# Kernel optimization log

Measured on AMD Instinct MI355X. Metric: run time of the kernel, lower is better.

The kernel has to match this reference:

```python
import jax, jax.numpy as jnp
import numpy as np

K = 20
EPS = 1e-5
NUM_CLASSES = 50


def knn_idx(x, k):
    # x: [B, C, N] -> [B, N, k] indices of k nearest neighbors (self included)
    xx = jnp.sum(x * x, axis=1)                      # [B, N]
    inner = jnp.einsum('bcn,bcm->bnm', x, x)         # [B, N, N]
    neg_dist = 2.0 * inner - xx[:, :, None] - xx[:, None, :]
    return jax.lax.top_k(neg_dist, k)[1]


def graph_feature(x, k):
    # x: [B, C, N] -> [B, 2C, N, k] edge features (feat - center, center)
    B = x.shape[0]
    idx = knn_idx(x, k)                              # [B, N, k]
    xt = jnp.transpose(x, (0, 2, 1))                 # [B, N, C]
    feat = xt[jnp.arange(B)[:, None, None], idx]     # [B, N, k, C]
    center = xt[:, :, None, :]
    out = jnp.concatenate([feat - center, jnp.broadcast_to(center, feat.shape)], axis=-1)
    return jnp.transpose(out, (0, 3, 1, 2))


def group_norm(x, groups, w, b):
    B, C = x.shape[0], x.shape[1]
    shp = x.shape
    xg = x.reshape(B, groups, -1)
    mu = jnp.mean(xg, axis=-1, keepdims=True)
    var = jnp.var(xg, axis=-1, keepdims=True)
    xn = ((xg - mu) * jax.lax.rsqrt(var + EPS)).reshape(shp)
    bshape = (1, C) + (1,) * (len(shp) - 2)
    return xn * w.reshape(bshape) + b.reshape(bshape)


def leaky(x):
    return jnp.where(x >= 0, x, 0.2 * x)


def edge_block(x, W, gw, gb, groups, k):
    f = graph_feature(x, k)                          # [B, 2C, N, k]
    h = jnp.einsum('oc,bcnk->bonk', W, f)            # 1x1 conv2d, no bias
    h = leaky(group_norm(h, groups, gw, gb))
    return jnp.max(h, axis=-1)                       # [B, Cout, N]


def conv1d(x, W, b):
    return jnp.einsum('oc,bcn->bon', W, x) + b[None, :, None]


def _mk(key, shape, fan_in):
    return jax.random.normal(key, shape, jnp.float32) * (1.0 / np.sqrt(fan_in))


def setup_inputs():
    key = jax.random.key(0)
    ks = jax.random.split(key, 32)
    B, N = 8, 2048
    d = {}
    d['x'] = jax.random.normal(ks[0], (B, 3, N), jnp.float32)
    d['W1'] = _mk(ks[1], (64, 6), 6)
    d['W2'] = _mk(ks[2], (64, 128), 128)
    d['W3'] = _mk(ks[3], (128, 128), 128)
    for i, (name, c) in enumerate([('g1', 64), ('g2', 64), ('g3', 128), ('gf', 1024), ('gs1', 512), ('gs2', 256), ('gs3', 128)]):
        d[name + 'w'] = 1.0 + 0.02 * jax.random.normal(ks[4 + 2 * i], (c,), jnp.float32)
        d[name + 'b'] = 0.02 * jax.random.normal(ks[5 + 2 * i], (c,), jnp.float32)
    d['Wm'] = _mk(ks[20], (1024, 256), 256)
    d['bm'] = jnp.zeros((1024,), jnp.float32)
    d['Ws1'] = _mk(ks[21], (512, 1280), 1280)
    d['bs1'] = jnp.zeros((512,), jnp.float32)
    d['Ws2'] = _mk(ks[22], (256, 512), 512)
    d['bs2'] = jnp.zeros((256,), jnp.float32)
    d['Ws3'] = _mk(ks[23], (128, 256), 256)
    d['bs3'] = jnp.zeros((128,), jnp.float32)
    d['Ws4'] = _mk(ks[24], (NUM_CLASSES, 128), 128)
    d['bs4'] = jnp.zeros((NUM_CLASSES,), jnp.float32)
    return d


def reference(x, W1, W2, W3, g1w, g1b, g2w, g2b, g3w, g3b, gfw, gfb, gs1w, gs1b, gs2w, gs2b, gs3w, gs3b, Wm, bm, Ws1, bs1, Ws2, bs2, Ws3, bs3, Ws4, bs4):
    B, _, N = x.shape
    x1 = edge_block(x, W1, g1w, g1b, 8, K)           # [B, 64, N]
    x2 = edge_block(x1, W2, g2w, g2b, 8, K)          # [B, 64, N]
    x3 = edge_block(x2, W3, g3w, g3b, 8, K)          # [B, 128, N]
    feats = jnp.concatenate([x1, x2, x3], axis=1)    # [B, 256, N]
    xb = jax.nn.relu(group_norm(conv1d(feats, Wm, bm), 32, gfw, gfb))  # [B, 1024, N]
    xmax = jnp.max(xb, axis=2)                       # [B, 1024]
    xmax_exp = jnp.broadcast_to(xmax[:, :, None], (B, 1024, N))
    combined = jnp.concatenate([xmax_exp, feats], axis=1)  # [B, 1280, N]
    h = jax.nn.relu(group_norm(conv1d(combined, Ws1, bs1), 16, gs1w, gs1b))
    h = jax.nn.relu(group_norm(conv1d(h, Ws2, bs2), 16, gs2w, gs2b))
    h = jax.nn.relu(group_norm(conv1d(h, Ws3, bs3), 8, gs3w, gs3b))
    logits = conv1d(h, Ws4, bs4)                     # [B, num_classes, N]
    return jax.nn.log_softmax(logits, axis=1)
```

## Files before the change

### kernel.cpp

```cpp
#include <hip/hip_runtime.h>

#define BN 8
#define NP 2048
#define KK 20
#define EPSV 1e-5f

typedef __attribute__((ext_vector_type(8))) short bf16x8;
typedef __attribute__((ext_vector_type(4))) float f32x4;

static __device__ __forceinline__ float leakyf(float v){ return v >= 0.f ? v : 0.2f*v; }
static __device__ __forceinline__ unsigned fenc(float f){
  unsigned u = __float_as_uint(f);
  unsigned m = (unsigned)((int)u >> 31);
  return u ^ (m | 0x80000000u);
}
static __device__ __forceinline__ float fdec(unsigned u){
  return __uint_as_float((u & 0x80000000u) ? (u & 0x7FFFFFFFu) : ~u);
}
static __device__ __forceinline__ unsigned bf2(float a, float b){
  unsigned ua = __float_as_uint(a), ub = __float_as_uint(b);
  ua = (ua + 0x7FFFu + ((ua>>16)&1u)) >> 16;
  ub = (ub + 0x7FFFu + ((ub>>16)&1u)) >> 16;
  return ua | (ub<<16);
}
static __device__ __forceinline__ unsigned short b16(float v){
  unsigned u = __float_as_uint(v);
  return (unsigned short)((u + 0x7FFFu + ((u>>16)&1u)) >> 16);
}
static __device__ __forceinline__ unsigned umax32(unsigned a, unsigned b){ return __builtin_elementwise_max(a,b); }
static __device__ __forceinline__ unsigned med3u(unsigned a, unsigned b, unsigned c){
  unsigned d;
  asm("v_med3_u32 %0, %1, %2, %3" : "=v"(d) : "v"(a), "v"(b), "v"(c));
  return d;
}

static __device__ __forceinline__ char* ldsW(char* base, int row, int colb){
  return base + row*80 + (colb ^ ((((unsigned)row>>3)&3u)<<4));
}
static __device__ __forceinline__ char* ldsX(char* base, int row, int colb){
  return base + row*80 + (colb ^ (((((unsigned)row>>2)^((unsigned)row>>4))&3u)<<4));
}
static __device__ __forceinline__ int swz128(int row, int colb){
  return (colb ^ ((row&7)<<4));
}

__global__ __launch_bounds__(256) void xx_kernel(const float* __restrict__ x, long ldb, int C,
                                                 float* __restrict__ xx){
  int b = blockIdx.y;
  int n = blockIdx.x*256 + threadIdx.x;
  const float* xp = x + (long)b*ldb + n;
  float a = 0.f;
  for(int c=0;c<C;c++){ float v = xp[(long)c*NP]; a += v*v; }
  xx[b*NP + n] = a;
}

static __device__ __forceinline__ void ins20(unsigned* tv, unsigned key){
  unsigned pold = tv[0];
  tv[0] = umax32(tv[0], key);
  #pragma unroll
  for(int r=1;r<20;r++){
    unsigned cold = tv[r];
    tv[r] = med3u(key, pold, cold);
    pold = cold;
  }
}

__global__ __launch_bounds__(256) void knnf_kernel(const unsigned short* __restrict__ fh,
                                                   const unsigned short* __restrict__ fl,
                                                   const float* __restrict__ xx,
                                                   unsigned* __restrict__ pk){
  __shared__ unsigned short CH[64][68];
  __shared__ unsigned short CL[64][68];
  __shared__ unsigned SK[64][68];
  __shared__ float cxs[64];
  const int b    = blockIdx.z;
  const int part = blockIdx.y;
  const int q0   = blockIdx.x*64;
  const int t    = threadIdx.x;
  const int lane = t & 63;
  const int w    = t >> 6;
  const int lr   = lane & 15, lg = lane >> 4;
  const unsigned short* fhb = fh + (long)b*NP*64;
  const unsigned short* flb = fl + (long)b*NP*64;
  const float* xxb = xx + b*NP;

  const unsigned short* qa = fhb + ((long)(q0 + w*16 + lr))*64 + lg*8;
  const unsigned short* qb = flb + ((long)(q0 + w*16 + lr))*64 + lg*8;
  bf16x8 ah0 = *(const bf16x8*)(qa);
  bf16x8 ah1 = *(const bf16x8*)(qa + 32);
  bf16x8 al0 = *(const bf16x8*)(qb);
  bf16x8 al1 = *(const bf16x8*)(qb + 32);
  float4 qxx4 = *(const float4*)(xxb + q0 + w*16 + lg*4);
  float qxx[4] = {qxx4.x, qxx4.y, qxx4.z, qxx4.w};

  unsigned tv[20];
  #pragma unroll
  for(int r=0;r<20;r++) tv[r] = 0u;
  const int sq = t>>2, sl = t&3;

  #define STAGE(ct_)                                                                  \
    {                                                                                 \
      const int ct__ = (ct_);                                                         \
      _Pragma("unroll")                                                               \
      for(int i = t; i < 512; i += 256){                                              \
        int row = i >> 3, seg = i & 7;                                                \
        *(uint4*)&CH[row][seg*8] = *(const uint4*)(fhb + ((long)(ct__*64+row))*64 + seg*8); \
        *(uint4*)&CL[row][seg*8] = *(const uint4*)(flb + ((long)(ct__*64+row))*64 + seg*8); \
      }                                                                               \
      if (t < 64) cxs[t] = xxb[ct__*64 + t];                                          \
    }

  STAGE(part*4);
  __syncthreads();

  #pragma unroll
  for(int cc=0; cc<4; cc++){
    __builtin_amdgcn_s_setprio(1);
    f32x4 acc[4];
    #pragma unroll
    for(int nt=0; nt<4; nt++){
      int crow = nt*16 + lr;
      bf16x8 bh0 = *(const bf16x8*)&CH[crow][lg*8];
      bf16x8 bh1 = *(const bf16x8*)&CH[crow][32 + lg*8];
      bf16x8 bl0 = *(const bf16x8*)&CL[crow][lg*8];
      bf16x8 bl1 = *(const bf16x8*)&CL[crow][32 + lg*8];
      f32x4 a = (f32x4){0.f,0.f,0.f,0.f};
      a = __builtin_amdgcn_mfma_f32_16x16x32_bf16(ah0, bh0, a, 0,0,0);
      a = __builtin_amdgcn_mfma_f32_16x16x32_bf16(ah1, bh1, a, 0,0,0);
      a = __builtin_amdgcn_mfma_f32_16x16x32_bf16(ah0, bl0, a, 0,0,0);
      a = __builtin_amdgcn_mfma_f32_16x16x32_bf16(ah1, bl1, a, 0,0,0);
      a = __builtin_amdgcn_mfma_f32_16x16x32_bf16(al0, bh0, a, 0,0,0);
      a = __builtin_amdgcn_mfma_f32_16x16x32_bf16(al1, bh1, a, 0,0,0);
      acc[nt] = a;
    }
    __builtin_amdgcn_s_setprio(0);
    float cxv[4];
    #pragma unroll
    for(int nt=0; nt<4; nt++) cxv[nt] = cxs[nt*16 + lr];
    unsigned key4[4][4];
    #pragma unroll
    for(int nt=0; nt<4; nt++){
      #pragma unroll
      for(int r=0;r<4;r++){
        float neg = 2.f*acc[nt][r] - qxx[r] - cxv[nt];
        key4[nt][r] = (fenc(neg) & 0xFFFFFF00u) | (255u - (unsigned)(cc*64 + nt*16 + lr));
      }
    }
    __syncthreads();
    #pragma unroll
    for(int nt=0; nt<4; nt++)
      #pragma unroll
      for(int r=0;r<4;r++)
        SK[w*16 + lg*4 + r][nt*16 + lr] = key4[nt][r];
    if (cc < 3){
      STAGE(part*4 + cc + 1);
    }
    __syncthreads();
    #pragma unroll
    for(int jj=0;jj<4;jj++){
      uint4 kv = *(const uint4*)&SK[sq][sl*16 + jj*4];
      ins20(tv, kv.x); ins20(tv, kv.y); ins20(tv, kv.z); ins20(tv, kv.w);
    }
  }
  #undef STAGE
  long base = ((((long)b*NP + q0 + sq)*8 + part)*4 + sl)*20;
  #pragma unroll
  for(int r=0;r<20;r++) pk[base+r] = tv[r];
}

__global__ __launch_bounds__(256) void knn1_kernel(const float* __restrict__ x,
                                                   const float* __restrict__ xx,
                                                   unsigned* __restrict__ pk){
  __shared__ float cx0[256], cx1[256], cx2[256], cxxa[256];
  const int b    = blockIdx.z;
  const int part = blockIdx.y;
  const int q0   = blockIdx.x*64;
  const int t    = threadIdx.x;
  const float* xb  = x + (long)b*3*NP;
  const float* xxb = xx + b*NP;

  cx0[t]  = xb[part*256 + t];
  cx1[t]  = xb[NP + part*256 + t];
  cx2[t]  = xb[2*NP + part*256 + t];
  cxxa[t] = xxb[part*256 + t];

  const int sq = t>>2, sl = t&3;
  const int q = q0 + sq;
  float qx = xb[q], qy = xb[NP + q], qz = xb[2*NP + q];
  float qxx = xxb[q];
  __syncthreads();

  unsigned tv[20];
  #pragma unroll
  for(int r=0;r<20;r++) tv[r] = 0u;

  for(int cc=0; cc<4; cc++){
    #pragma unroll
    for(int j=0;j<16;j++){
      int m = cc*64 + sl*16 + j;
      float ip = qx*cx0[m] + qy*cx1[m] + qz*cx2[m];
      float neg = 2.f*ip - qxx - cxxa[m];
      unsigned key = (fenc(neg) & 0xFFFFFF00u) | (255u - (unsigned)m);
      ins20(tv, key);
    }
  }
  long base = ((((long)b*NP + q0 + sq)*8 + part)*4 + sl)*20;
  #pragma unroll
  for(int r=0;r<20;r++) pk[base+r] = tv[r];
}

__global__ __launch_bounds__(256) void knnmerge_kernel(const unsigned* __restrict__ pk,
                                                       int* __restrict__ idxout){
  const int wid  = threadIdx.x >> 6;
  const int lane = threadIdx.x & 63;
  const long qg = (long)blockIdx.x*4 + wid;
  const unsigned* kb = pk + qg*640;
  const int l = lane >> 1, h = lane & 1;
  unsigned k[10];
  {
    const unsigned* src = kb + l*20 + h*10;
    #pragma unroll
    for(int i=0;i<10;i++) k[i] = src[i];
  }
  int rem = 10;
  int* op = idxout + qg*KK;
  const int gbase = (l>>2)*256;
  for(int r=0;r<KK;r++){
    unsigned key = k[0];
    int gi = gbase + 255 - (int)(key & 255u);
    unsigned long long cmp = (rem > 0)
        ? ((unsigned long long)(key & 0xFFFFFF00u) << 32) | (unsigned)(0x7FFFFFFF - gi)
        : 0ull;
    unsigned long long w = cmp;
    #pragma unroll
    for(int s=1;s<64;s<<=1){
      unsigned long long o = __shfl_xor(w, s, 64);
      w = (o > w) ? o : w;
    }
    if (lane == 0){
      op[r] = 0x7FFFFFFF - (int)(unsigned)(w & 0xFFFFFFFFu);
    }
    if (cmp == w){
      #pragma unroll
      for(int i=0;i<9;i++) k[i] = k[i+1];
      rem--;
    }
  }
}

template<int CIN, int O>
__global__ __launch_bounds__(256) void pcdual_kernel(const float* __restrict__ x, long ldb,
                                                     const float* __restrict__ W,
                                                     float* __restrict__ ya, float* __restrict__ dd){
  __shared__ float Wt[CIN][O+1];
  constexpr int NLOC = 256/O;
  const int b = blockIdx.y;
  const int n0 = blockIdx.x*NLOC;
  const int t = threadIdx.x;
  const int o = t % O;
  const int n = n0 + t/O;
  const float* xp = x + (long)b*ldb + n;
  float xv[CIN];
  #pragma unroll
  for(int c=0;c<CIN;c++) xv[c] = xp[(long)c*NP];
  for(int i=t;i<CIN*O;i+=256){ int oo=i/CIN, c=i%CIN; Wt[c][oo] = W[(long)oo*2*CIN + c]; }
  __syncthreads();
  float aa = 0.f;
  #pragma unroll
  for(int c=0;c<CIN;c++) aa += Wt[c][o]*xv[c];
  __syncthreads();
  for(int i=t;i<CIN*O;i+=256){ int oo=i/CIN, c=i%CIN; Wt[c][oo] = W[(long)oo*2*CIN + CIN + c]; }
  __syncthreads();
  float ab = 0.f;
  #pragma unroll
  for(int c=0;c<CIN;c++) ab += Wt[c][o]*xv[c];
  long outoff = ((long)b*NP + n)*O + o;
  ya[outoff] = aa;
  dd[outoff] = ab - aa;
}

template<int O>
__global__ __launch_bounds__(256) void pcdualm_kernel(const unsigned short* __restrict__ fh,
                                                      const unsigned short* __restrict__ fl,
                                                      const float* __restrict__ W,
                                                      float* __restrict__ ya, float* __restrict__ dd){
  __shared__ unsigned short AH[O][64];
  __shared__ unsigned short AL[O][64];
  __shared__ unsigned short DH[O][64];
  __shared__ unsigned short DL[O][64];
  const int b  = blockIdx.y;
  const int n0 = blockIdx.x*64;
  const int t  = threadIdx.x;
  const int lane = t & 63;
  const int w  = t >> 6;
  const int lr = lane & 15, lg = lane >> 4;

  for(int i=t; i<O*64; i+=256){
    int o = i >> 6, c = i & 63;
    float va = W[(long)o*128 + c];
    float vb = W[(long)o*128 + 64 + c];
    float vd = vb - va;
    unsigned short ah = b16(va);
    unsigned short dh = b16(vd);
    int byt = swz128(o, c*2);
    *(unsigned short*)((char*)&AH[o][0] + byt) = ah;
    *(unsigned short*)((char*)&AL[o][0] + byt) = b16(va - __uint_as_float(((unsigned)ah)<<16));
    *(unsigned short*)((char*)&DH[o][0] + byt) = dh;
    *(unsigned short*)((char*)&DL[o][0] + byt) = b16(vd - __uint_as_float(((unsigned)dh)<<16));
  }

  const int n = n0 + w*16 + lr;
  const unsigned short* xh = fh + ((long)b*NP + n)*64 + lg*8;
  const unsigned short* xl = fl + ((long)b*NP + n)*64 + lg*8;
  bf16x8 xh0 = *(const bf16x8*)(xh);
  bf16x8 xh1 = *(const bf16x8*)(xh + 32);
  bf16x8 xl0 = *(const bf16x8*)(xl);
  bf16x8 xl1 = *(const bf16x8*)(xl + 32);
  __syncthreads();

  #pragma unroll
  for(int mi=0; mi<O/16; mi++){
    int row = mi*16 + lr;
    bf16x8 a_h0 = *(const bf16x8*)((char*)&AH[row][0] + swz128(row, lg*16));
    bf16x8 a_h1 = *(const bf16x8*)((char*)&AH[row][0] + swz128(row, 64 + lg*16));
    bf16x8 a_l0 = *(const bf16x8*)((char*)&AL[row][0] + swz128(row, lg*16));
    bf16x8 a_l1 = *(const bf16x8*)((char*)&AL[row][0] + swz128(row, 64 + lg*16));
    f32x4 aa = (f32x4){0.f,0.f,0.f,0.f};
    aa = __builtin_amdgcn_mfma_f32_16x16x32_bf16(a_h0, xh0, aa, 0,0,0);
    aa = __builtin_amdgcn_mfma_f32_16x16x32_bf16(a_h1, xh1, aa, 0,0,0);
    aa = __builtin_amdgcn_mfma_f32_16x16x32_bf16(a_h0, xl0, aa, 0,0,0);
    aa = __builtin_amdgcn_mfma_f32_16x16x32_bf16(a_h1, xl1, aa, 0,0,0);
    aa = __builtin_amdgcn_mfma_f32_16x16x32_bf16(a_l0, xh0, aa, 0,0,0);
    aa = __builtin_amdgcn_mfma_f32_16x16x32_bf16(a_l1, xh1, aa, 0,0,0);
    bf16x8 d_h0 = *(const bf16x8*)((char*)&DH[row][0] + swz128(row, lg*16));
    bf16x8 d_h1 = *(const bf16x8*)((char*)&DH[row][0] + swz128(row, 64 + lg*16));
    bf16x8 d_l0 = *(const bf16x8*)((char*)&DL[row][0] + swz128(row, lg*16));
    bf16x8 d_l1 = *(const bf16x8*)((char*)&DL[row][0] + swz128(row, 64 + lg*16));
    f32x4 ad = (f32x4){0.f,0.f,0.f,0.f};
    ad = __builtin_amdgcn_mfma_f32_16x16x32_bf16(d_h0, xh0, ad, 0,0,0);
    ad = __builtin_amdgcn_mfma_f32_16x16x32_bf16(d_h1, xh1, ad, 0,0,0);
    ad = __builtin_amdgcn_mfma_f32_16x16x32_bf16(d_h0, xl0, ad, 0,0,0);
    ad = __builtin_amdgcn_mfma_f32_16x16x32_bf16(d_h1, xl1, ad, 0,0,0);
    ad = __builtin_amdgcn_mfma_f32_16x16x32_bf16(d_l0, xh0, ad, 0,0,0);
    ad = __builtin_amdgcn_mfma_f32_16x16x32_bf16(d_l1, xh1, ad, 0,0,0);
    long ooff = ((long)b*NP + n)*O + mi*16 + lg*4;
    float4 va = {aa[0],aa[1],aa[2],aa[3]};
    float4 vd = {ad[0],ad[1],ad[2],ad[3]};
    *(float4*)(ya + ooff) = va;
    *(float4*)(dd + ooff) = vd;
  }
}

template<int O>
__global__ __launch_bounds__(256) void egather_kernel(const float* __restrict__ ya, const float* __restrict__ dd,
                               const int* __restrict__ idx,
                               float* __restrict__ mx, float* __restrict__ mn,
                               float* __restrict__ stats){
  __shared__ float sred2[4][16];
  constexpr int NSUB = 256/O;
  constexpr int CPG = O/8;
  const int b  = blockIdx.x & 7;
  const int n0 = (blockIdx.x >> 3) * 32;
  const int t = threadIdx.x;
  const int w = t >> 6;
  const int o = t % O;
  const int ns = t / O;
  if (t < 64) sred2[t>>4][t&15] = 0.f;
  __syncthreads();
  float gs = 0.f, gs2 = 0.f;
  const float* yab = ya + (long)b*NP*O;
  for(int p=ns; p<32; p+=NSUB){
    int n = n0 + p;
    float d = dd[((long)b*NP + n)*O + o];
    const int* ip = idx + ((long)b*NP + n)*KK;
    float m = -__builtin_inff(), mm = __builtin_inff(), s = 0.f, s2 = 0.f;
    #pragma unroll
    for(int k=0;k<KK;k++){
      int j = ip[k];
      float v = yab[(long)j*O + o] + d;
      s += v; s2 += v*v;
      m = fmaxf(m, v); mm = fminf(mm, v);
    }
    mx[((long)b*NP + n)*O + o] = m;
    mn[((long)b*NP + n)*O + o] = mm;
    gs += s; gs2 += s2;
  }
  #pragma unroll
  for(int offm=1; offm<CPG; offm<<=1){
    gs  += __shfl_xor(gs,  offm, CPG);
    gs2 += __shfl_xor(gs2, offm, CPG);
  }
  if ((o & (CPG-1)) == 0){
    int g = o / CPG;
    sred2[w][g*2]   = gs;
    sred2[w][g*2+1] = gs2;
  }
  __syncthreads();
  if (t < 16){
    float a = sred2[0][t] + sred2[1][t] + sred2[2][t] + sred2[3][t];
    atomicAdd(&stats[b*16 + t], a);
  }
}

template<int O, bool NEEDXX, bool WRITEH>
__global__ __launch_bounds__(256) void enorm_kernel(const float* __restrict__ mx, const float* __restrict__ mn,
                                                    const float* __restrict__ stats,
                                                    const float* __restrict__ gw, const float* __restrict__ gb,
                                                    float* __restrict__ feats, int coff,
                                                    float* __restrict__ xxout,
                                                    unsigned* __restrict__ fhout, unsigned* __restrict__ flout){
  __shared__ float lmx[64][65];
  __shared__ float lmn[64][65];
  const int b = blockIdx.z;
  const int o0 = blockIdx.y*64;
  const int n0 = blockIdx.x*64;
  const int t = threadIdx.x;
  for(int r=0;r<16;r++){
    int i = r*4 + t/64, j = t%64;
    long src = ((long)b*NP + n0 + i)*O + o0 + j;
    lmx[i][j] = mx[src];
    lmn[i][j] = mn[src];
  }
  __syncthreads();
  constexpr int CPG = O/8;
  const float inv_cnt = 1.f/((float)CPG*NP*KK);
  float xacc = 0.f;
  for(int r=0;r<16;r++){
    int ol = r*4 + t/64, nl = t%64;
    int og = o0 + ol;
    int g = og / CPG;
    float S  = stats[(b*8+g)*2];
    float S2 = stats[(b*8+g)*2+1];
    float mu = S*inv_cnt;
    float var = S2*inv_cnt - mu*mu;
    float rs = rsqrtf(var + EPSV);
    float w = gw[og], bb = gb[og];
    float sel = (w >= 0.f) ? lmx[nl][ol] : lmn[nl][ol];
    float v = leakyf((sel - mu)*rs*w + bb);
    feats[((long)b*256 + coff + og)*NP + n0 + nl] = v;
    if (WRITEH) lmx[nl][ol] = v;
    if (NEEDXX) xacc += v*v;
  }
  if (WRITEH){
    __syncthreads();
    #pragma unroll
    for(int k=0;k<8;k++){
      int flat = k*256 + t;
      int n = flat >> 5, cp = flat & 31;
      float v0 = lmx[n][2*cp], v1 = lmx[n][2*cp+1];
      unsigned short h0 = b16(v0), h1 = b16(v1);
      float r0 = v0 - __uint_as_float(((unsigned)h0)<<16);
      float r1 = v1 - __uint_as_float(((unsigned)h1)<<16);
      unsigned short l0 = b16(r0), l1 = b16(r1);
      long o = ((long)b*NP + n0 + n)*32 + cp;
      fhout[o] = (unsigned)h0 | ((unsigned)h1<<16);
      flout[o] = (unsigned)l0 | ((unsigned)l1<<16);
    }
  }
  if (NEEDXX){
    __syncthreads();
    float* red = &lmx[0][0];
    red[(t>>6)*64 + (t&63)] = xacc;
    __syncthreads();
    if (t < 64){
      float a = red[t] + red[64+t] + red[128+t] + red[192+t];
      xxout[b*NP + n0 + t] = a;
    }
  }
}

template<bool WRITE_Y, bool DO_STATS, bool DO_MAXMIN, bool IN_NORM>
__global__ __launch_bounds__(256) void mgemm_kernel(
    const float* __restrict__ W, int ldw,
    const float* __restrict__ x, long xldb,
    const float* __restrict__ bias, const float* __restrict__ basev,
    int O, int C, int gshift,
    float* __restrict__ y, float* __restrict__ stats,
    unsigned* __restrict__ mmax, unsigned* __restrict__ mmin,
    const float* __restrict__ instats, const float* __restrict__ igw,
    const float* __restrict__ igb, int igshift, float iinv)
{
  __shared__ __align__(16) char WlB[128*80];
  __shared__ __align__(16) char XtB[128*80];
  __shared__ float sred[16];
  __shared__ unsigned smax[128];
  __shared__ unsigned smin[128];

  const int b  = blockIdx.z;
  const int o0 = blockIdx.y*128;
  const int nb = blockIdx.x*128;
  const int t  = threadIdx.x;
  const int lane = t & 63;
  const int wid = t >> 6;
  const int wmo = wid >> 1, wno = wid & 1;
  const int lr = lane & 15, lg = lane >> 4;

  if (DO_STATS && t < 16) sred[t] = 0.f;
  if (DO_MAXMIN && t < 128){ smax[t] = 0u; smin[t] = 0xFFFFFFFFu; }

  f32x4 acc[4][4];
  #pragma unroll
  for(int i=0;i<4;i++)
    #pragma unroll
    for(int j=0;j<4;j++) acc[i][j] = (f32x4){0.f,0.f,0.f,0.f};

  const int so  = t & 127;
  const int scb = (t >> 7) << 5;
  const int xcg = t >> 5;
  const int xng = t & 31;

  for(int cc=0; cc<C; cc+=32){
    __syncthreads();
    {
      const float* wp = W + (long)(o0 + so)*ldw + cc + (scb>>1);
      #pragma unroll
      for(int j=0;j<4;j++){
        float4 f = *(const float4*)(wp + j*4);
        uint2 v = { bf2(f.x,f.y), bf2(f.z,f.w) };
        *(uint2*)ldsW(WlB, so, scb + j*8) = v;
      }
    }
    {
      const float* xp = x + (long)b*xldb + (long)(cc + xcg*4)*NP + nb + xng*4;
      float4 f0 = *(const float4*)(xp);
      float4 f1 = *(const float4*)(xp + NP);
      float4 f2 = *(const float4*)(xp + 2*NP);
      float4 f3 = *(const float4*)(xp + 3*NP);
      float X4[4][4] = {{f0.x,f0.y,f0.z,f0.w},{f1.x,f1.y,f1.z,f1.w},
                        {f2.x,f2.y,f2.z,f2.w},{f3.x,f3.y,f3.z,f3.w}};
      if (IN_NORM){
        #pragma unroll
        for(int i=0;i<4;i++){
          int c = cc + xcg*4 + i;
          int g = c >> igshift;
          const float* sp = instats + ((long)b*(C>>igshift) + g)*2;
          float mu = sp[0]*iinv;
          float var = sp[1]*iinv - mu*mu;
          float rs = rsqrtf(var + EPSV);
          float aa = rs*igw[c];
          float c2 = igb[c] - mu*aa;
          #pragma unroll
          for(int j=0;j<4;j++) X4[i][j] = fmaxf(X4[i][j]*aa + c2, 0.f);
        }
      }
      #pragma unroll
      for(int j=0;j<4;j++){
        uint2 v = { bf2(X4[0][j], X4[1][j]), bf2(X4[2][j], X4[3][j]) };
        *(uint2*)ldsX(XtB, xng*4 + j, xcg*8) = v;
      }
    }
    __syncthreads();
    bf16x8 afr[4], bfr[4];
    #pragma unroll
    for(int mi=0;mi<4;mi++) afr[mi] = *(const bf16x8*)ldsW(WlB, wmo*64 + mi*16 + lr, lg*16);
    #pragma unroll
    for(int nj=0;nj<4;nj++) bfr[nj] = *(const bf16x8*)ldsX(XtB, wno*64 + nj*16 + lr, lg*16);
    #pragma unroll
    for(int mi=0;mi<4;mi++)
      #pragma unroll
      for(int nj=0;nj<4;nj++)
        acc[mi][nj] = __builtin_amdgcn_mfma_f32_16x16x32_bf16(afr[mi], bfr[nj], acc[mi][nj], 0, 0, 0);
  }

  float bb4[4][4];
  #pragma unroll
  for(int mi=0;mi<4;mi++){
    #pragma unroll
    for(int r=0;r<4;r++){
      int o = o0 + wmo*64 + mi*16 + lg*4 + r;
      float v = 0.f;
      if (bias)  v += bias[o];
      if (basev) v += basev[(long)b*O + o];
      bb4[mi][r] = v;
    }
  }
  #pragma unroll
  for(int mi=0;mi<4;mi++)
    #pragma unroll
    for(int nj=0;nj<4;nj++)
      #pragma unroll
      for(int r=0;r<4;r++) acc[mi][nj][r] += bb4[mi][r];

  if (WRITE_Y){
    #pragma unroll
    for(int mi=0;mi<4;mi++)
      #pragma unroll
      for(int nj=0;nj<4;nj++)
        #pragma unroll
        for(int r=0;r<4;r++){
          int o = o0 + wmo*64 + mi*16 + lg*4 + r;
          y[((long)b*O + o)*NP + nb + wno*64 + nj*16 + lr] = acc[mi][nj][r];
        }
  }
  if (DO_STATS){
    #pragma unroll
    for(int mi=0;mi<4;mi++){
      float s = 0.f, s2 = 0.f;
      #pragma unroll
      for(int nj=0;nj<4;nj++)
        #pragma unroll
        for(int r=0;r<4;r++){ float v = acc[mi][nj][r]; s += v; s2 += v*v; }
      int gi = (wmo*64 + mi*16) >> gshift;
      atomicAdd(&sred[gi*2],   s);
      atomicAdd(&sred[gi*2+1], s2);
    }
  }
  if (DO_MAXMIN){
    #pragma unroll
    for(int mi=0;mi<4;mi++)
      #pragma unroll
      for(int r=0;r<4;r++){
        float mv = acc[mi][0][r], mw = acc[mi][0][r];
        #pragma unroll
        for(int nj=1;nj<4;nj++){ mv = fmaxf(mv, acc[mi][nj][r]); mw = fminf(mw, acc[mi][nj][r]); }
        int ol = wmo*64 + mi*16 + lg*4 + r;
        atomicMax(&smax[ol], fenc(mv));
        atomicMin(&smin[ol], fenc(mw));
      }
  }
  if (DO_STATS || DO_MAXMIN) __syncthreads();
  if (DO_STATS){
    int ngb = 128 >> gshift;
    if (t < ngb*2){
      atomicAdd(&stats[((long)b*(O>>gshift) + (o0>>gshift) + (t>>1))*2 + (t&1)], sred[t]);
    }
  }
  if (DO_MAXMIN){
    if (t < 128){
      atomicMax(&mmax[(long)b*O + o0 + t], smax[t]);
      atomicMin(&mmin[(long)b*O + o0 + t], smin[t]);
    }
  }
}

__global__ void xmax_kernel(const unsigned* __restrict__ mmax, const unsigned* __restrict__ mmin,
                            const float* __restrict__ stats, const float* __restrict__ gw,
                            const float* __restrict__ gb, float* __restrict__ xmax){
  int t = blockIdx.x*256 + threadIdx.x;
  int b = t >> 10, o = t & 1023;
  int g = o >> 5;
  const float* sp = stats + (b*32+g)*2;
  const float inv_cnt = 1.f/(32.f*NP);
  float mu = sp[0]*inv_cnt;
  float var = sp[1]*inv_cnt - mu*mu;
  float rs = rsqrtf(var + EPSV);
  float w = gw[o];
  float sel = (w >= 0.f) ? fdec(mmax[t]) : fdec(mmin[t]);
  float v = (sel - mu)*rs*w + gb[o];
  xmax[t] = fmaxf(v, 0.f);
}

__global__ __launch_bounds__(256) void base1_kernel(const float* __restrict__ Ws1, const float* __restrict__ bs1,
                                                    const float* __restrict__ xmax, float* __restrict__ base1){
  __shared__ float sred[4][8];
  const int o = blockIdx.x;
  const int t = threadIdx.x;
  const float* wp = Ws1 + (long)o*1280;
  float acc[8];
  #pragma unroll
  for(int bb=0;bb<8;bb++) acc[bb]=0.f;
  #pragma unroll
  for(int cc=0;cc<4;cc++){
    int c = cc*256 + t;
    float w = wp[c];
    #pragma unroll
    for(int bb=0;bb<8;bb++) acc[bb] += w * xmax[bb*1024 + c];
  }
  #pragma unroll
  for(int bb=0;bb<8;bb++){
    float a = acc[bb];
    a += __shfl_xor(a,1);  a += __shfl_xor(a,2);  a += __shfl_xor(a,4);
    a += __shfl_xor(a,8);  a += __shfl_xor(a,16); a += __shfl_xor(a,32);
    acc[bb]=a;
  }
  if ((t&63)==0){
    #pragma unroll
    for(int bb=0;bb<8;bb++) sred[t>>6][bb]=acc[bb];
  }
  __syncthreads();
  if (t<8){
    float a = sred[0][t]+sred[1][t]+sred[2][t]+sred[3][t] + bs1[o];
    base1[t*512 + o] = a;
  }
}

__global__ __launch_bounds__(256) void s4_kernel(const float* __restrict__ h3raw,
                                                 const float* __restrict__ stats,
                                                 const float* __restrict__ gw, const float* __restrict__ gb,
                                                 const float* __restrict__ W,
                                                 const float* __restrict__ bias,
                                                 float* __restrict__ out){
  const int b = blockIdx.y;
  const int n = blockIdx.x*64 + (threadIdx.x>>2);
  const int cl = threadIdx.x & 3;
  const float inv_cnt = 1.f/(16.f*NP);
  float mu0, rs0, mu1, rs1;
  {
    const float* sp = stats + (b*8 + cl*2)*2;
    mu0 = sp[0]*inv_cnt;
    float var = sp[1]*inv_cnt - mu0*mu0;
    rs0 = rsqrtf(var + EPSV);
    const float* sp1 = stats + (b*8 + cl*2 + 1)*2;
    mu1 = sp1[0]*inv_cnt;
    float var1 = sp1[1]*inv_cnt - mu1*mu1;
    rs1 = rsqrtf(var1 + EPSV);
  }
  float hv[32];
  #pragma unroll
  for(int c=0;c<32;c++){
    int og = cl*32 + c;
    float rs = (c < 16) ? rs0 : rs1;
    float mu = (c < 16) ? mu0 : mu1;
    float a = rs*gw[og];
    float c2 = gb[og] - mu*a;
    float v = h3raw[((long)b*128 + og)*NP + n];
    hv[c] = fmaxf(v*a + c2, 0.f);
  }
  float zz[50];
  #pragma unroll
  for(int o=0;o<50;o++){
    const float* wp = W + o*128 + cl*32;
    float a = 0.f;
    #pragma unroll
    for(int c=0;c<32;c++) a += wp[c]*hv[c];
    a += __shfl_xor(a,1);
    a += __shfl_xor(a,2);
    zz[o] = a + bias[o];
  }
  float m = zz[0];
  #pragma unroll
  for(int o=1;o<50;o++) m = fmaxf(m, zz[o]);
  float s = 0.f;
  #pragma unroll
  for(int o=0;o<50;o++) s += __expf(zz[o]-m);
  float lse = m + __logf(s);
  #pragma unroll
  for(int o=0;o<50;o++){
    if ((o&3)==cl) out[((long)b*50+o)*NP+n] = zz[o]-lse;
  }
}

extern "C" void kernel_launch(void* const* d_in, const int* in_sizes, int n_in,
                              void* d_out, int out_size, void* d_ws, size_t ws_size,
                              hipStream_t stream)
{
  const float* x   = (const float*)d_in[0];
  const float* W1  = (const float*)d_in[1];
  const float* W2  = (const float*)d_in[2];
  const float* W3  = (const float*)d_in[3];
  const float* g1w = (const float*)d_in[4];
  const float* g1b = (const float*)d_in[5];
  const float* g2w = (const float*)d_in[6];
  const float* g2b = (const float*)d_in[7];
  const float* g3w = (const float*)d_in[8];
  const float* g3b = (const float*)d_in[9];
  const float* gfw = (const float*)d_in[10];
  const float* gfb = (const float*)d_in[11];
  const float* gs1w= (const float*)d_in[12];
  const float* gs1b= (const float*)d_in[13];
  const float* gs2w= (const float*)d_in[14];
  const float* gs2b= (const float*)d_in[15];
  const float* gs3w= (const float*)d_in[16];
  const float* gs3b= (const float*)d_in[17];
  const float* Wm  = (const float*)d_in[18];
  const float* bm  = (const float*)d_in[19];
  const float* Ws1 = (const float*)d_in[20];
  const float* bs1 = (const float*)d_in[21];
  const float* Ws2 = (const float*)d_in[22];
  const float* bs2 = (const float*)d_in[23];
  const float* Ws3 = (const float*)d_in[24];
  const float* bs3 = (const float*)d_in[25];
  const float* Ws4 = (const float*)d_in[26];
  const float* bs4 = (const float*)d_in[27];
  float* out = (float*)d_out;

  char* ws = (char*)d_ws;
  size_t off = 0;
  auto alloc = [&](size_t bytes)->char*{
    char* p = ws + off;
    off += (bytes + 255) & ~(size_t)255;
    return p;
  };
  char* zbase = alloc(6656 + 32768);
  float* estats1 = (float*)(zbase + 0);
  float* estats2 = (float*)(zbase + 512);
  float* estats3 = (float*)(zbase + 1024);
  float* mstats  = (float*)(zbase + 1536);
  float* s1stats = (float*)(zbase + 3584);
  float* s2stats = (float*)(zbase + 4608);
  float* s3stats = (float*)(zbase + 5632);
  unsigned* mmax = (unsigned*)(zbase + 6656);
  unsigned* mmin = (unsigned*)alloc(32768);
  float* xmaxb = (float*)alloc(8*1024*4);
  float* base1 = (float*)alloc(8*512*4);
  float* feats = (float*)alloc((size_t)BN*256*NP*4);
  int*   idxb  = (int*)  alloc((size_t)BN*NP*KK*4);
  float* xxb   = (float*)alloc((size_t)BN*NP*4);
  unsigned* fhb = (unsigned*)alloc((size_t)BN*NP*64*2);
  unsigned* flb = (unsigned*)alloc((size_t)BN*NP*64*2);
  float* ya    = (float*)alloc((size_t)BN*NP*128*4);
  float* dd    = (float*)alloc((size_t)BN*NP*128*4);
  float* mx    = (float*)alloc((size_t)BN*NP*128*4);
  float* mn    = (float*)alloc((size_t)BN*NP*128*4);
  float* ybuf1 = (float*)alloc((size_t)BN*512*NP*4);
  float* ybuf2 = (float*)alloc((size_t)BN*256*NP*4);
  float* ybuf3 = (float*)alloc((size_t)BN*128*NP*4);

  unsigned* pk = (unsigned*)ya;
  const unsigned short* fh16 = (const unsigned short*)fhb;
  const unsigned short* fl16 = (const unsigned short*)flb;

  hipMemsetAsync(zbase, 0, 6656 + 32768, stream);
  hipMemsetAsync(mmin, 0xFF, 32768, stream);

  dim3 blk256(256);

  xx_kernel<<<dim3(NP/256, BN), blk256, 0, stream>>>(x, (long)3*NP, 3, xxb);
  knn1_kernel<<<dim3(NP/64, 8, BN), blk256, 0, stream>>>(x, xxb, pk);
  knnmerge_kernel<<<dim3(BN*NP/4), blk256, 0, stream>>>(pk, idxb);
  pcdual_kernel<3,64><<<dim3(NP/4, BN), blk256, 0, stream>>>(x, (long)3*NP, W1, ya, dd);
  egather_kernel<64><<<dim3(8*NP/32), blk256, 0, stream>>>(ya, dd, idxb, mx, mn, estats1);
  enorm_kernel<64,true,true><<<dim3(NP/64, 1, BN), blk256, 0, stream>>>(
      mx, mn, estats1, g1w, g1b, feats, 0, xxb, fhb, flb);

  knnf_kernel<<<dim3(NP/64, 8, BN), blk256, 0, stream>>>(fh16, fl16, xxb, pk);
  knnmerge_kernel<<<dim3(BN*NP/4), blk256, 0, stream>>>(pk, idxb);
  pcdualm_kernel<64><<<dim3(NP/64, BN), blk256, 0, stream>>>(fh16, fl16, W2, ya, dd);
  egather_kernel<64><<<dim3(8*NP/32), blk256, 0, stream>>>(ya, dd, idxb, mx, mn, estats2);
  enorm_kernel<64,true,true><<<dim3(NP/64, 1, BN), blk256, 0, stream>>>(
      mx, mn, estats2, g2w, g2b, feats, 64, xxb, fhb, flb);

  knnf_kernel<<<dim3(NP/64, 8, BN), blk256, 0, stream>>>(fh16, fl16, xxb, pk);
  knnmerge_kernel<<<dim3(BN*NP/4), blk256, 0, stream>>>(pk, idxb);
  pcdualm_kernel<128><<<dim3(NP/64, BN), blk256, 0, stream>>>(fh16, fl16, W3, ya, dd);
  egather_kernel<128><<<dim3(8*NP/32), blk256, 0, stream>>>(ya, dd, idxb, mx, mn, estats3);
  enorm_kernel<128,false,false><<<dim3(NP/64, 2, BN), blk256, 0, stream>>>(
      mx, mn, estats3, g3w, g3b, feats, 128, nullptr, nullptr, nullptr);

  mgemm_kernel<false,true,true,false><<<dim3(16,8,BN), blk256, 0, stream>>>(
      Wm, 256, feats, (long)256*NP, bm, nullptr, 1024, 256, 5,
      nullptr, mstats, mmax, mmin, nullptr, nullptr, nullptr, 0, 0.f);
  xmax_kernel<<<dim3(32), blk256, 0, stream>>>(mmax, mmin, mstats, gfw, gfb, xmaxb);
  base1_kernel<<<dim3(512), blk256, 0, stream>>>(Ws1, bs1, xmaxb, base1);

  mgemm_kernel<true,true,false,false><<<dim3(16,4,BN), blk256, 0, stream>>>(
      Ws1 + 1024, 1280, feats, (long)256*NP, nullptr, base1, 512, 256, 5,
      ybuf1, s1stats, nullptr, nullptr, nullptr, nullptr, nullptr, 0, 0.f);

  mgemm_kernel<true,true,false,true><<<dim3(16,2,BN), blk256, 0, stream>>>(
      Ws2, 512, ybuf1, (long)512*NP, bs2, nullptr, 256, 512, 4,
      ybuf2, s2stats, nullptr, nullptr, s1stats, gs1w, gs1b, 5, 1.f/(32.f*NP));

  mgemm_kernel<true,true,false,true><<<dim3(16,1,BN), blk256, 0, stream>>>(
      Ws3, 256, ybuf2, (long)256*NP, bs3, nullptr, 128, 256, 4,
      ybuf3, s3stats, nullptr, nullptr, s2stats, gs2w, gs2b, 4, 1.f/(16.f*NP));

  s4_kernel<<<dim3(NP/64, BN), blk256, 0, stream>>>(ybuf3, s3stats, gs3w, gs3b, Ws4, bs4, out);
}
```

Baseline: 535.9 us.

## Store concatenated features as point-major bf16 and feed GEMMs directly from it

Removes the fp32 channel-major feats buffer. Edge-block outputs are written only into a point-major bf16 hi buffer with 256 channels per point, plus a lo buffer for the first 128 channels. The kNN and pointwise kernels read this buffer at a channel offset. The first two mgemm launches load B fragments straight from global bf16 instead of staging fp32 through LDS, which cuts conversion, LDS traffic and memory footprint. The trade-off is that mgemm operands become single bf16 (no lo part) and the global fragment loads are strided.

```diff
diff --git a/kernel.cpp b/kernel.cpp
--- a/kernel.cpp
+++ b/kernel.cpp
@@ -67,6 +67,7 @@
 
 __global__ __launch_bounds__(256) void knnf_kernel(const unsigned short* __restrict__ fh,
                                                    const unsigned short* __restrict__ fl,
+                                                   int cbase,
                                                    const float* __restrict__ xx,
                                                    unsigned* __restrict__ pk){
   __shared__ unsigned short CH[64][68];
@@ -80,12 +81,12 @@
   const int lane = t & 63;
   const int w    = t >> 6;
   const int lr   = lane & 15, lg = lane >> 4;
-  const unsigned short* fhb = fh + (long)b*NP*64;
-  const unsigned short* flb = fl + (long)b*NP*64;
+  const unsigned short* fhb = fh + (long)b*NP*256;
+  const unsigned short* flb = fl + (long)b*NP*128;
   const float* xxb = xx + b*NP;
 
-  const unsigned short* qa = fhb + ((long)(q0 + w*16 + lr))*64 + lg*8;
-  const unsigned short* qb = flb + ((long)(q0 + w*16 + lr))*64 + lg*8;
+  const unsigned short* qa = fhb + ((long)(q0 + w*16 + lr))*256 + cbase + lg*8;
+  const unsigned short* qb = flb + ((long)(q0 + w*16 + lr))*128 + cbase + lg*8;
   bf16x8 ah0 = *(const bf16x8*)(qa);
   bf16x8 ah1 = *(const bf16x8*)(qa + 32);
   bf16x8 al0 = *(const bf16x8*)(qb);
@@ -98,16 +99,16 @@
   for(int r=0;r<20;r++) tv[r] = 0u;
   const int sq = t>>2, sl = t&3;
 
-  #define STAGE(ct_)                                                                  \
-    {                                                                                 \
-      const int ct__ = (ct_);                                                         \
-      _Pragma("unroll")                                                               \
-      for(int i = t; i < 512; i += 256){                                              \
-        int row = i >> 3, seg = i & 7;                                                \
-        *(uint4*)&CH[row][seg*8] = *(const uint4*)(fhb + ((long)(ct__*64+row))*64 + seg*8); \
-        *(uint4*)&CL[row][seg*8] = *(const uint4*)(flb + ((long)(ct__*64+row))*64 + seg*8); \
-      }                                                                               \
-      if (t < 64) cxs[t] = xxb[ct__*64 + t];                                          \
+  #define STAGE(ct_)                                                                        \
+    {                                                                                       \
+      const int ct__ = (ct_);                                                               \
+      _Pragma("unroll")                                                                     \
+      for(int i = t; i < 512; i += 256){                                                    \
+        int row = i >> 3, seg = i & 7;                                                      \
+        *(uint4*)&CH[row][seg*8] = *(const uint4*)(fhb + ((long)(ct__*64+row))*256 + cbase + seg*8); \
+        *(uint4*)&CL[row][seg*8] = *(const uint4*)(flb + ((long)(ct__*64+row))*128 + cbase + seg*8); \
+      }                                                                                     \
+      if (t < 64) cxs[t] = xxb[ct__*64 + t];                                                \
     }
 
   STAGE(part*4);
@@ -282,6 +283,7 @@
 template<int O>
 __global__ __launch_bounds__(256) void pcdualm_kernel(const unsigned short* __restrict__ fh,
                                                       const unsigned short* __restrict__ fl,
+                                                      int cbase,
                                                       const float* __restrict__ W,
                                                       float* __restrict__ ya, float* __restrict__ dd){
   __shared__ unsigned short AH[O][64];
@@ -310,8 +312,8 @@
   }
 
   const int n = n0 + w*16 + lr;
-  const unsigned short* xh = fh + ((long)b*NP + n)*64 + lg*8;
-  const unsigned short* xl = fl + ((long)b*NP + n)*64 + lg*8;
+  const unsigned short* xh = fh + ((long)b*NP + n)*256 + cbase + lg*8;
+  const unsigned short* xl = fl + ((long)b*NP + n)*128 + cbase + lg*8;
   bf16x8 xh0 = *(const bf16x8*)(xh);
   bf16x8 xh1 = *(const bf16x8*)(xh + 32);
   bf16x8 xl0 = *(const bf16x8*)(xl);
@@ -402,11 +404,11 @@
   }
 }
 
-template<int O, bool NEEDXX, bool WRITEH>
+template<int O, bool NEEDXX, bool WRITEL>
 __global__ __launch_bounds__(256) void enorm_kernel(const float* __restrict__ mx, const float* __restrict__ mn,
                                                     const float* __restrict__ stats,
                                                     const float* __restrict__ gw, const float* __restrict__ gb,
-                                                    float* __restrict__ feats, int coff,
+                                                    int coff,
                                                     float* __restrict__ xxout,
                                                     unsigned* __restrict__ fhout, unsigned* __restrict__ flout){
   __shared__ float lmx[64][65];
@@ -437,29 +439,30 @@
     float w = gw[og], bb = gb[og];
     float sel = (w >= 0.f) ? lmx[nl][ol] : lmn[nl][ol];
     float v = leakyf((sel - mu)*rs*w + bb);
-    feats[((long)b*256 + coff + og)*NP + n0 + nl] = v;
-    if (WRITEH) lmx[nl][ol] = v;
+    lmx[nl][ol] = v;
     if (NEEDXX) xacc += v*v;
   }
-  if (WRITEH){
-    __syncthreads();
+  __syncthreads();
+  {
+    const int cb2 = (coff + o0) >> 1;
     #pragma unroll
     for(int k=0;k<8;k++){
       int flat = k*256 + t;
       int n = flat >> 5, cp = flat & 31;
       float v0 = lmx[n][2*cp], v1 = lmx[n][2*cp+1];
       unsigned short h0 = b16(v0), h1 = b16(v1);
-      float r0 = v0 - __uint_as_float(((unsigned)h0)<<16);
-      float r1 = v1 - __uint_as_float(((unsigned)h1)<<16);
-      unsigned short l0 = b16(r0), l1 = b16(r1);
-      long o = ((long)b*NP + n0 + n)*32 + cp;
-      fhout[o] = (unsigned)h0 | ((unsigned)h1<<16);
-      flout[o] = (unsigned)l0 | ((unsigned)l1<<16);
+      fhout[((long)b*NP + n0 + n)*128 + cb2 + cp] = (unsigned)h0 | ((unsigned)h1<<16);
+      if (WRITEL){
+        float r0 = v0 - __uint_as_float(((unsigned)h0)<<16);
+        float r1 = v1 - __uint_as_float(((unsigned)h1)<<16);
+        flout[((long)b*NP + n0 + n)*64 + cb2 + cp] =
+            (unsigned)b16(r0) | ((unsigned)b16(r1)<<16);
+      }
     }
   }
   if (NEEDXX){
     __syncthreads();
-    float* red = &lmx[0][0];
+    float* red = &lmn[0][0];
     red[(t>>6)*64 + (t&63)] = xacc;
     __syncthreads();
     if (t < 64){
@@ -469,10 +472,11 @@
   }
 }
 
-template<bool WRITE_Y, bool DO_STATS, bool DO_MAXMIN, bool IN_NORM>
+template<bool WRITE_Y, bool DO_STATS, bool DO_MAXMIN, bool IN_NORM, bool XBF16>
 __global__ __launch_bounds__(256) void mgemm_kernel(
     const float* __restrict__ W, int ldw,
     const float* __restrict__ x, long xldb,
+    const unsigned short* __restrict__ xbf,
     const float* __restrict__ bias, const float* __restrict__ basev,
     int O, int C, int gshift,
     float* __restrict__ y, float* __restrict__ stats,
@@ -481,7 +485,7 @@
     const float* __restrict__ igb, int igshift, float iinv)
 {
   __shared__ __align__(16) char WlB[128*80];
-  __shared__ __align__(16) char XtB[128*80];
+  __shared__ __align__(16) char XtB[XBF16 ? 16 : 128*80];
   __shared__ float sred[16];
   __shared__ unsigned smax[128];
   __shared__ unsigned smin[128];
@@ -510,6 +514,12 @@
   const int xng = t & 31;
 
   for(int cc=0; cc<C; cc+=32){
+    bf16x8 bfr[4];
+    if (XBF16){
+      #pragma unroll
+      for(int nj=0;nj<4;nj++)
+        bfr[nj] = *(const bf16x8*)(xbf + ((long)b*NP + nb + wno*64 + nj*16 + lr)*256 + cc + lg*8);
+    }
     __syncthreads();
     {
       const float* wp = W + (long)(o0 + so)*ldw + cc + (scb>>1);
@@ -520,7 +530,7 @@
         *(uint2*)ldsW(WlB, so, scb + j*8) = v;
       }
     }
-    {
+    if (!XBF16){
       const float* xp = x + (long)b*xldb + (long)(cc + xcg*4)*NP + nb + xng*4;
       float4 f0 = *(const float4*)(xp);
       float4 f1 = *(const float4*)(xp + NP);
@@ -550,11 +560,13 @@
       }
     }
     __syncthreads();
-    bf16x8 afr[4], bfr[4];
+    bf16x8 afr[4];
     #pragma unroll
     for(int mi=0;mi<4;mi++) afr[mi] = *(const bf16x8*)ldsW(WlB, wmo*64 + mi*16 + lr, lg*16);
-    #pragma unroll
-    for(int nj=0;nj<4;nj++) bfr[nj] = *(const bf16x8*)ldsX(XtB, wno*64 + nj*16 + lr, lg*16);
+    if (!XBF16){
+      #pragma unroll
+      for(int nj=0;nj<4;nj++) bfr[nj] = *(const bf16x8*)ldsX(XtB, wno*64 + nj*16 + lr, lg*16);
+    }
     #pragma unroll
     for(int mi=0;mi<4;mi++)
       #pragma unroll
@@ -793,11 +805,10 @@
   unsigned* mmin = (unsigned*)alloc(32768);
   float* xmaxb = (float*)alloc(8*1024*4);
   float* base1 = (float*)alloc(8*512*4);
-  float* feats = (float*)alloc((size_t)BN*256*NP*4);
   int*   idxb  = (int*)  alloc((size_t)BN*NP*KK*4);
   float* xxb   = (float*)alloc((size_t)BN*NP*4);
-  unsigned* fhb = (unsigned*)alloc((size_t)BN*NP*64*2);
-  unsigned* flb = (unsigned*)alloc((size_t)BN*NP*64*2);
+  unsigned* fhb = (unsigned*)alloc((size_t)BN*NP*256*2);
+  unsigned* flb = (unsigned*)alloc((size_t)BN*NP*128*2);
   float* ya    = (float*)alloc((size_t)BN*NP*128*4);
   float* dd    = (float*)alloc((size_t)BN*NP*128*4);
   float* mx    = (float*)alloc((size_t)BN*NP*128*4);
@@ -821,38 +832,38 @@
   pcdual_kernel<3,64><<<dim3(NP/4, BN), blk256, 0, stream>>>(x, (long)3*NP, W1, ya, dd);
   egather_kernel<64><<<dim3(8*NP/32), blk256, 0, stream>>>(ya, dd, idxb, mx, mn, estats1);
   enorm_kernel<64,true,true><<<dim3(NP/64, 1, BN), blk256, 0, stream>>>(
-      mx, mn, estats1, g1w, g1b, feats, 0, xxb, fhb, flb);
-
-  knnf_kernel<<<dim3(NP/64, 8, BN), blk256, 0, stream>>>(fh16, fl16, xxb, pk);
+      mx, mn, estats1, g1w, g1b, 0, xxb, fhb, flb);
+
+  knnf_kernel<<<dim3(NP/64, 8, BN), blk256, 0, stream>>>(fh16, fl16, 0, xxb, pk);
   knnmerge_kernel<<<dim3(BN*NP/4), blk256, 0, stream>>>(pk, idxb);
-  pcdualm_kernel<64><<<dim3(NP/64, BN), blk256, 0, stream>>>(fh16, fl16, W2, ya, dd);
+  pcdualm_kernel<64><<<dim3(NP/64, BN), blk256, 0, stream>>>(fh16, fl16, 0, W2, ya, dd);
   egather_kernel<64><<<dim3(8*NP/32), blk256, 0, stream>>>(ya, dd, idxb, mx, mn, estats2);
   enorm_kernel<64,true,true><<<dim3(NP/64, 1, BN), blk256, 0, stream>>>(
-      mx, mn, estats2, g2w, g2b, feats, 64, xxb, fhb, flb);
-
-  knnf_kernel<<<dim3(NP/64, 8, BN), blk256, 0, stream>>>(fh16, fl16, xxb, pk);
+      mx, mn, estats2, g2w, g2b, 64, xxb, fhb, flb);
+
+  knnf_kernel<<<dim3(NP/64, 8, BN), blk256, 0, stream>>>(fh16, fl16, 64, xxb, pk);
   knnmerge_kernel<<<dim3(BN*NP/4), blk256, 0, stream>>>(pk, idxb);
-  pcdualm_kernel<128><<<dim3(NP/64, BN), blk256, 0, stream>>>(fh16, fl16, W3, ya, dd);
+  pcdualm_kernel<128><<<dim3(NP/64, BN), blk256, 0, stream>>>(fh16, fl16, 64, W3, ya, dd);
   egather_kernel<128><<<dim3(8*NP/32), blk256, 0, stream>>>(ya, dd, idxb, mx, mn, estats3);
   enorm_kernel<128,false,false><<<dim3(NP/64, 2, BN), blk256, 0, stream>>>(
-      mx, mn, estats3, g3w, g3b, feats, 128, nullptr, nullptr, nullptr);
-
-  mgemm_kernel<false,true,true,false><<<dim3(16,8,BN), blk256, 0, stream>>>(
-      Wm, 256, feats, (long)256*NP, bm, nullptr, 1024, 256, 5,
+      mx, mn, estats3, g3w, g3b, 128, nullptr, fhb, nullptr);
+
+  mgemm_kernel<false,true,true,false,true><<<dim3(16,8,BN), blk256, 0, stream>>>(
+      Wm, 256, nullptr, 0, fh16, bm, nullptr, 1024, 256, 5,
       nullptr, mstats, mmax, mmin, nullptr, nullptr, nullptr, 0, 0.f);
   xmax_kernel<<<dim3(32), blk256, 0, stream>>>(mmax, mmin, mstats, gfw, gfb, xmaxb);
   base1_kernel<<<dim3(512), blk256, 0, stream>>>(Ws1, bs1, xmaxb, base1);
 
-  mgemm_kernel<true,true,false,false><<<dim3(16,4,BN), blk256, 0, stream>>>(
-      Ws1 + 1024, 1280, feats, (long)256*NP, nullptr, base1, 512, 256, 5,
+  mgemm_kernel<true,true,false,false,true><<<dim3(16,4,BN), blk256, 0, stream>>>(
+      Ws1 + 1024, 1280, nullptr, 0, fh16, nullptr, base1, 512, 256, 5,
       ybuf1, s1stats, nullptr, nullptr, nullptr, nullptr, nullptr, 0, 0.f);
 
-  mgemm_kernel<true,true,false,true><<<dim3(16,2,BN), blk256, 0, stream>>>(
-      Ws2, 512, ybuf1, (long)512*NP, bs2, nullptr, 256, 512, 4,
+  mgemm_kernel<true,true,false,true,false><<<dim3(16,2,BN), blk256, 0, stream>>>(
+      Ws2, 512, ybuf1, (long)512*NP, nullptr, bs2, nullptr, 256, 512, 4,
       ybuf2, s2stats, nullptr, nullptr, s1stats, gs1w, gs1b, 5, 1.f/(32.f*NP));
 
-  mgemm_kernel<true,true,false,true><<<dim3(16,1,BN), blk256, 0, stream>>>(
-      Ws3, 256, ybuf2, (long)256*NP, bs3, nullptr, 128, 256, 4,
+  mgemm_kernel<true,true,false,true,false><<<dim3(16,1,BN), blk256, 0, stream>>>(
+      Ws3, 256, ybuf2, (long)256*NP, nullptr, bs3, nullptr, 128, 256, 4,
       ybuf3, s3stats, nullptr, nullptr, s2stats, gs2w, gs2b, 4, 1.f/(16.f*NP));
 
   s4_kernel<<<dim3(NP/64, BN), blk256, 0, stream>>>(ybuf3, s3stats, gs3w, gs3b, Ws4, bs4, out);
```

Result: slower. 546.7 us (+2.0%).
